# Kernel optimization log

Hardware: AMD Instinct MI355X
Metric: run time of the kernel (lower is better)

Reference implementation:

```python
import jax, jax.numpy as jnp
import numpy as np
import math

# Constants from module defaults
NUM_HEADS = 16
STEEP = 10.0        # SpikeFunction surrogate steepness
LEAK = 0.9          # LIF leak_rate
THRESH = 1.0        # spike_threshold
REFRAC = 2.0        # refractory_period
TH_DECAY = 0.95     # adaptive threshold decay

@jax.custom_vjp
def spike_fn(v, th):
    return (v >= th).astype(v.dtype)

def _spike_fwd(v, th):
    return spike_fn(v, th), (v, th)

def _spike_bwd(res, g):
    v, th = res
    s = jax.nn.sigmoid(STEEP * (v - th))
    return (g * STEEP * s * (1.0 - s), jnp.zeros_like(th))

spike_fn.defvjp(_spike_fwd, _spike_bwd)


def lif(cur_seq, W_rec, theta):
    """Leaky integrate-and-fire recurrence.
    cur_seq: [S, N, Dh] precomputed input currents (input_weights applied already).
    Returns spikes [S, N, Dh]."""
    S, N, Dh = cur_seq.shape
    dt = cur_seq.dtype
    init = (jnp.zeros((N, Dh), dt),               # membrane potential
            jnp.zeros((N, Dh), dt),               # spike history (detached)
            jnp.zeros((N, Dh), dt),               # refractory counter
            jnp.full((N, Dh), THRESH, dt))        # adaptive threshold

    def step(state, cur):
        v, hist, refrac, athr = state
        total = cur + hist @ W_rec.T
        v = LEAK * v + total
        v = v * (refrac <= 0).astype(dt)          # refractory masking
        spikes = spike_fn(v, athr)
        sm = jax.lax.stop_gradient(spikes)        # spike_mask (bool in torch, no grad)
        v = v * (1.0 - sm)                        # membrane reset
        refrac = jnp.maximum(refrac - 1.0, sm * REFRAC)
        athr = TH_DECAY * athr + sm * theta       # adaptive threshold bump
        return (v, sm, refrac, athr), spikes

    _, spikes = jax.lax.scan(step, init, cur_seq)
    return spikes


def setup_inputs() -> dict:
    key = jax.random.key(0)
    B, S, D = 4, 1024, 1024
    H = NUM_HEADS
    Dh = D // H
    ks = jax.random.split(key, 16)
    sD = 1.0 / math.sqrt(D)
    sd = 1.0 / math.sqrt(Dh)
    inp = {
        "x": jax.random.normal(ks[0], (B, S, D), jnp.float32),
        "Wq": jax.random.normal(ks[1], (D, D), jnp.float32) * sD,
        "Wk": jax.random.normal(ks[2], (D, D), jnp.float32) * sD,
        "Wv": jax.random.normal(ks[3], (D, D), jnp.float32) * sD,
        "Wo": jax.random.normal(ks[4], (D, D), jnp.float32) * sD,
        "bo": jax.random.normal(ks[5], (D,), jnp.float32) * sD,
        "Wq_in": jax.random.normal(ks[6], (Dh, Dh), jnp.float32) * sd,
        "Wq_rec": jax.random.normal(ks[7], (Dh, Dh), jnp.float32) * sd,
        "Wk_in": jax.random.normal(ks[8], (Dh, Dh), jnp.float32) * sd,
        "Wk_rec": jax.random.normal(ks[9], (Dh, Dh), jnp.float32) * sd,
        "Wv_in": jax.random.normal(ks[10], (Dh, Dh), jnp.float32) * sd,
        "Wv_rec": jax.random.normal(ks[11], (Dh, Dh), jnp.float32) * sd,
        "theta_q": jnp.full((Dh,), 0.1, jnp.float32),
        "theta_k": jnp.full((Dh,), 0.1, jnp.float32),
        "theta_v": jnp.full((Dh,), 0.1, jnp.float32),
    }
    return inp


def reference(x, Wq, Wk, Wv, Wo, bo, Wq_in, Wq_rec, Wk_in, Wk_rec,
              Wv_in, Wv_rec, theta_q, theta_k, theta_v):
    B, S, D = x.shape
    H = NUM_HEADS
    Dh = D // H

    def heads_time_major(t):
        # [B,S,D] -> [S, B*H, Dh]
        return t.reshape(B, S, H, Dh).transpose(1, 0, 2, 3).reshape(S, B * H, Dh)

    # Projections; LIF input current is linear so apply input_weights over whole seq
    cur_q = heads_time_major(x @ Wq.T) @ Wq_in.T
    cur_k = heads_time_major(x @ Wk.T) @ Wk_in.T
    cur_v = heads_time_major(x @ Wv.T) @ Wv_in.T

    qs = lif(cur_q, Wq_rec, theta_q)
    ks_ = lif(cur_k, Wk_rec, theta_k)
    vs = lif(cur_v, Wv_rec, theta_v)

    def back(t):
        # [S, B*H, Dh] -> [B, H, S, Dh]
        return t.reshape(S, B, H, Dh).transpose(1, 2, 0, 3)

    qh, kh, vh = back(qs), back(ks_), back(vs)
    scale = 1.0 / math.sqrt(Dh)
    scores = jnp.einsum('bhqd,bhkd->bhqk', qh, kh) * scale
    attn = jax.nn.softmax(scores, axis=-1)
    ctx = jnp.einsum('bhqk,bhkd->bhqd', attn, vh)
    out = ctx.transpose(0, 2, 1, 3).reshape(B, S, D) @ Wo.T + bo
    return out
```

## Files before the change

### kernel.cpp

```cpp
#include <hip/hip_runtime.h>
#include <hip/hip_bf16.h>

#define B_  4
#define S_  1024
#define D_  1024
#define H_  16
#define DH_ 64
#define N_  64
#define BS_ 4096

#define WS_CUR   0ull
#define WS_XH    (WS_CUR + 48ull*1024*1024)
#define WS_XL    (WS_XH  +  8ull*1024*1024)
#define WS_WCH   (WS_XL  +  8ull*1024*1024)
#define WS_WCL   (WS_WCH +  6ull*1024*1024)
#define WS_MSK   (WS_WCL +  6ull*1024*1024)
#define WS_CTXH  WS_XH
#define WS_CTXL  WS_XL
#define WS_WOH   WS_WCH
#define WS_WOL   (WS_WCH + 2ull*1024*1024)

typedef __attribute__((ext_vector_type(8))) short short8v;
typedef __attribute__((ext_vector_type(4))) float f32x4;

__device__ inline void bsplit(float x, unsigned short& h, unsigned short& l) {
    unsigned ux = __float_as_uint(x);
    unsigned rh = (ux + 0x7FFFu + ((ux >> 16) & 1u)) >> 16;
    h = (unsigned short)rh;
    float r = x - __uint_as_float(rh << 16);
    unsigned ur = __float_as_uint(r);
    l = (unsigned short)((ur + 0x7FFFu + ((ur >> 16) & 1u)) >> 16);
}

__global__ __launch_bounds__(256) void k_prep(
    const float* __restrict__ x,
    const float* __restrict__ Wq, const float* __restrict__ Wk, const float* __restrict__ Wv,
    const float* __restrict__ Wqi, const float* __restrict__ Wki, const float* __restrict__ Wvi,
    unsigned short* __restrict__ xh, unsigned short* __restrict__ xl,
    unsigned short* __restrict__ wch, unsigned short* __restrict__ wcl)
{
    int blk = blockIdx.x;
    int tid = threadIdx.x;

    if (blk < 4096) {
        int i = (blk * 256 + tid) * 4;
        float4 v = *reinterpret_cast<const float4*>(&x[i]);
        ushort4 h, l;
        bsplit(v.x, h.x, l.x);
        bsplit(v.y, h.y, l.y);
        bsplit(v.z, h.z, l.z);
        bsplit(v.w, h.w, l.w);
        *reinterpret_cast<ushort4*>(&xh[i]) = h;
        *reinterpret_cast<ushort4*>(&xl[i]) = l;
        return;
    }

    int q = blk - 4096;
    int z = q >> 10, hd = q & 1023;
    const float* W  = (z == 0) ? Wq  : (z == 1) ? Wk  : Wv;
    const float* Wi = (z == 0) ? Wqi : (z == 1) ? Wki : Wvi;
    int h = hd >> 6, d = hd & 63;

    __shared__ float ws[64];
    if (tid < 64) ws[tid] = Wi[d * 64 + tid];
    __syncthreads();

    const float* Wb = W + (size_t)h * 64 * 1024;
    float acc[4] = {0.f, 0.f, 0.f, 0.f};
    for (int j = 0; j < 64; j++) {
        float wv = ws[j];
        const float* row = Wb + (size_t)j * 1024;
        #pragma unroll
        for (int mi = 0; mi < 4; mi++)
            acc[mi] += row[tid + mi * 256] * wv;
    }
    unsigned short* oh = wch + (size_t)z * 1024 * 1024 + (size_t)hd * 1024;
    unsigned short* ol = wcl + (size_t)z * 1024 * 1024 + (size_t)hd * 1024;
    #pragma unroll
    for (int mi = 0; mi < 4; mi++) {
        unsigned short hh, ll;
        bsplit(acc[mi], hh, ll);
        oh[tid + mi * 256] = hh;
        ol[tid + mi * 256] = ll;
    }
}

template<int OUT>
__global__ __launch_bounds__(512, 4) void k_mfma_gemm(
    const unsigned short* __restrict__ Ah, const unsigned short* __restrict__ Al,
    const unsigned short* __restrict__ Bh, const unsigned short* __restrict__ Bl,
    float* __restrict__ C, const float* __restrict__ bias)
{
    __shared__ __align__(16) unsigned short lds[4 * 128 * 64];

    int tid = threadIdx.x;
    int bx = blockIdx.x, by = blockIdx.y, bz = blockIdx.z;
    const unsigned short* Bhz = Bh + (size_t)bz * 1024 * 1024;
    const unsigned short* Blz = Bl + (size_t)bz * 1024 * 1024;
    int rb = bx * 128, cb = by * 128;

    int wid = tid >> 6, lane = tid & 63;
    int wr = wid >> 2, wc = wid & 3;
    int r15 = lane & 15, g = lane >> 4;

    int rowA = lane >> 3;
    int kpsw = ((lane & 7) ^ rowA) * 8;

    f32x4 acc[4][2];
    #pragma unroll
    for (int mt = 0; mt < 4; mt++)
        #pragma unroll
        for (int nt = 0; nt < 2; nt++)
            acc[mt][nt] = (f32x4){0.f, 0.f, 0.f, 0.f};

    #pragma unroll 1
    for (int t = 0; t < 16; t++) {
        int kb = t * 64;
        #pragma unroll
        for (int i = 0; i < 8; i++) {
            int q = wid * 8 + i;
            int mat = q >> 4, ch = q & 15;
            const unsigned short* gsrc = (mat == 0) ? Ah : (mat == 1) ? Al
                                        : (mat == 2) ? Bhz : Blz;
            int rowoff = (mat < 2) ? rb : cb;
            int row = ch * 8 + rowA;
            __builtin_amdgcn_global_load_lds(
                (const __attribute__((address_space(1))) void*)
                    (gsrc + (size_t)(rowoff + row) * 1024 + kb + kpsw),
                (__attribute__((address_space(3))) void*)(&lds[mat * 8192 + ch * 512]),
                16, 0, 0);
        }
        __syncthreads();

        #pragma unroll
        for (int kk = 0; kk < 2; kk++) {
            short8v bh[2], bl[2];
            #pragma unroll
            for (int nt = 0; nt < 2; nt++) {
                int Crow = wc * 32 + nt * 16 + r15;
                int off = Crow * 64 + (((kk * 4 + g) ^ (Crow & 7)) * 8);
                bh[nt] = *reinterpret_cast<const short8v*>(&lds[2 * 8192 + off]);
                bl[nt] = *reinterpret_cast<const short8v*>(&lds[3 * 8192 + off]);
            }
            #pragma unroll
            for (int mt = 0; mt < 4; mt++) {
                int Arow = wr * 64 + mt * 16 + r15;
                int off = Arow * 64 + (((kk * 4 + g) ^ (Arow & 7)) * 8);
                short8v ah = *reinterpret_cast<const short8v*>(&lds[0 * 8192 + off]);
                short8v al = *reinterpret_cast<const short8v*>(&lds[1 * 8192 + off]);
                #pragma unroll
                for (int nt = 0; nt < 2; nt++) {
                    acc[mt][nt] = __builtin_amdgcn_mfma_f32_16x16x32_bf16(bh[nt], ah, acc[mt][nt], 0, 0, 0);
                    acc[mt][nt] = __builtin_amdgcn_mfma_f32_16x16x32_bf16(bl[nt], ah, acc[mt][nt], 0, 0, 0);
                    acc[mt][nt] = __builtin_amdgcn_mfma_f32_16x16x32_bf16(bh[nt], al, acc[mt][nt], 0, 0, 0);
                }
            }
        }
        __syncthreads();
    }

    if (OUT == 0) {
        float* out = C + (size_t)bz * 64 * 1024 * 64;
        int b = rb >> 10;
        #pragma unroll
        for (int nt = 0; nt < 2; nt++) {
            int col = cb + wc * 32 + nt * 16 + g * 4;
            int h = col >> 6, dd = col & 63;
            #pragma unroll
            for (int mt = 0; mt < 4; mt++) {
                int row = rb + wr * 64 + mt * 16 + r15;
                int s = row & 1023;
                f32x4 a = acc[mt][nt];
                *reinterpret_cast<float4*>(&out[(((size_t)(b * 16 + h)) * 1024 + s) * 64 + dd]) =
                    make_float4(a[0], a[1], a[2], a[3]);
            }
        }
    } else {
        #pragma unroll
        for (int nt = 0; nt < 2; nt++) {
            int col = cb + wc * 32 + nt * 16 + g * 4;
            float4 bv = *reinterpret_cast<const float4*>(&bias[col]);
            #pragma unroll
            for (int mt = 0; mt < 4; mt++) {
                int row = rb + wr * 64 + mt * 16 + r15;
                f32x4 a = acc[mt][nt];
                *reinterpret_cast<float4*>(&C[(size_t)row * 1024 + col]) =
                    make_float4(a[0] + bv.x, a[1] + bv.y, a[2] + bv.z, a[3] + bv.w);
            }
        }
    }
}

__global__ __launch_bounds__(64) void k_lif_wo(
    const float* __restrict__ curAll,
    const float* __restrict__ Wrq, const float* __restrict__ Wrk, const float* __restrict__ Wrv,
    const float* __restrict__ thq, const float* __restrict__ thk, const float* __restrict__ thv,
    unsigned long long* __restrict__ masks,
    const float* __restrict__ Wo, unsigned short* __restrict__ woh, unsigned short* __restrict__ wol)
{
    __shared__ float T[16 * 16 * 64];
    __shared__ __align__(16) float cbuf[2][64 * 64];

    int bid = blockIdx.x;
    int d = threadIdx.x;

    if (bid >= 192) {
        int q = bid - 192;
        #pragma unroll
        for (int it = 0; it < 8; it++) {
            int i = q * 2048 + it * 256 + d * 4;
            float4 v = *reinterpret_cast<const float4*>(&Wo[i]);
            ushort4 h, l;
            bsplit(v.x, h.x, l.x);
            bsplit(v.y, h.y, l.y);
            bsplit(v.z, h.z, l.z);
            bsplit(v.w, h.w, l.w);
            *reinterpret_cast<ushort4*>(&woh[i]) = h;
            *reinterpret_cast<ushort4*>(&wol[i]) = l;
        }
        return;
    }

    int l = bid >> 6, n = bid & 63;
    const float* W  = (l == 0) ? Wrq : (l == 1) ? Wrk : Wrv;
    const float* th = (l == 0) ? thq : (l == 1) ? thk : thv;
    const float* cbase = curAll + (((size_t)l * 64 + n) * 1024) * 64;
    unsigned long long* mout = masks + ((size_t)l * 64 + n) * 1024;

    #pragma unroll
    for (int j = 0; j < 16; j++)
        __builtin_amdgcn_global_load_lds(
            (const __attribute__((address_space(1))) void*)(cbase + j * 256 + d * 4),
            (__attribute__((address_space(3))) void*)(&cbuf[0][j * 256]), 16, 0, 0);

    float theta = th[d];

    for (int g = 0; g < 16; g++) {
        float w0 = W[d * 64 + 4 * g + 0];
        float w1 = W[d * 64 + 4 * g + 1];
        float w2 = W[d * 64 + 4 * g + 2];
        float w3 = W[d * 64 + 4 * g + 3];
        #pragma unroll
        for (int c = 0; c < 16; c++) {
            float t = 0.f;
            if (c & 1) t += w0;
            if (c & 2) t += w1;
            if (c & 4) t += w2;
            if (c & 8) t += w3;
            T[g * 1024 + c * 64 + d] = t;
        }
    }
    __syncthreads();

    float v = 0.f, refrac = 0.f, athr = 1.0f;
    unsigned mlo = 0u, mhi = 0u;
    unsigned bufLo = 0u, bufHi = 0u;

    for (int b = 0; b < 16; b++) {
        if (b < 15) {
            const float* src = cbase + (size_t)(b + 1) * 4096;
            float* dst = cbuf[(b + 1) & 1];
            #pragma unroll
            for (int j = 0; j < 16; j++)
                __builtin_amdgcn_global_load_lds(
                    (const __attribute__((address_space(1))) void*)(src + j * 256 + d * 4),
                    (__attribute__((address_space(3))) void*)(dst + j * 256), 16, 0, 0);
        }
        if (b == 0)      asm volatile("s_waitcnt vmcnt(16)" ::: "memory");
        else if (b < 15) asm volatile("s_waitcnt vmcnt(17)" ::: "memory");
        else             asm volatile("s_waitcnt vmcnt(0)"  ::: "memory");

        const float* cb = cbuf[b & 1];
        #pragma unroll 8
        for (int i = 0; i < 64; i++) {
            float curv = cb[i * 64 + d];

            float t[16];
            #pragma unroll
            for (int g = 0; g < 8; g++)
                t[g] = T[g * 1024 + (int)(((mlo >> (4 * g)) & 15u) << 6) + d];
            #pragma unroll
            for (int g = 0; g < 8; g++)
                t[8 + g] = T[(8 + g) * 1024 + (int)(((mhi >> (4 * g)) & 15u) << 6) + d];

            #pragma unroll
            for (int k = 8; k >= 1; k >>= 1)
                #pragma unroll
                for (int j = 0; j < k; j++)
                    t[j] = t[j] + t[j + k];
            float total = curv + t[0];

            v = 0.9f * v + total;
            v = (refrac <= 0.f) ? v : 0.f;
            bool sp = (v >= athr);
            unsigned long long m = __ballot(sp);
            mlo = (unsigned)m;
            mhi = (unsigned)(m >> 32);
            bufLo = (d == i) ? mlo : bufLo;
            bufHi = (d == i) ? mhi : bufHi;
            float sm = sp ? 1.f : 0.f;
            v = sp ? 0.f : v;
            refrac = fmaxf(refrac - 1.f, sm * 2.f);
            athr = 0.95f * athr + sm * theta;
        }
        mout[b * 64 + d] = ((unsigned long long)bufHi << 32) | bufLo;
    }
}

#define ATT_C1 0.180336879f
#define ATT_C2 11.541560327f

__device__ inline short8v expand8(unsigned byte) {
    short8v r;
    #pragma unroll
    for (int e = 0; e < 8; e++)
        r[e] = (short)(((byte >> e) & 1u) ? 0x3F80 : 0);
    return r;
}

__device__ inline unsigned bfpk(float x, float y) {
    unsigned ux = __float_as_uint(x);
    unsigned uy = __float_as_uint(y);
    unsigned rx = (ux + 0x7FFFu + ((ux >> 16) & 1u)) >> 16;
    unsigned ry = (uy + 0x7FFFu + ((uy >> 16) & 1u)) >> 16;
    return rx | (ry << 16);
}

__global__ __launch_bounds__(256) void k_attn_mfma(
    const unsigned long long* __restrict__ masks,
    unsigned short* __restrict__ ctxh, unsigned short* __restrict__ ctxl)
{
    __shared__ __align__(16) unsigned short Klds[128][72];
    __shared__ __align__(16) unsigned short Vt[64][136];
    __shared__ unsigned long long vmbuf[2][128];

    const unsigned long long* qm_all = masks;
    const unsigned long long* km_all = masks + (size_t)64 * 1024;
    const unsigned long long* vm_all = masks + (size_t)2 * 64 * 1024;

    int n  = blockIdx.y;
    int qc = blockIdx.x;
    int tid = threadIdx.x;
    int wv = tid >> 6;
    int lane = tid & 63;
    int r15 = lane & 15, g = lane >> 4;

    const unsigned long long* km = km_all + (size_t)n * 1024;
    const unsigned long long* vm = vm_all + (size_t)n * 1024;

    unsigned long long qmask = qm_all[(size_t)n * 1024 + qc * 64 + wv * 16 + r15];
    short8v Qf[2];
    #pragma unroll
    for (int ch = 0; ch < 2; ch++)
        Qf[ch] = expand8((unsigned)(qmask >> ((ch * 4 + g) * 8)) & 0xFFu);

    f32x4 cx[4];
    #pragma unroll
    for (int mt = 0; mt < 4; mt++) cx[mt] = (f32x4){0.f, 0.f, 0.f, 0.f};
    float den = 0.f;

    if (tid < 128) vmbuf[0][tid] = vm[tid];
    __syncthreads();

    for (int kt = 0; kt < 8; kt++) {
        {
            int s = tid >> 1, half = tid & 1;
            unsigned long long m = km[kt * 128 + s];
            #pragma unroll
            for (int j = 0; j < 4; j++) {
                unsigned byte = (unsigned)(m >> (half * 32 + j * 8)) & 0xFFu;
                *reinterpret_cast<short8v*>(&Klds[s][(half * 4 + j) * 8]) = expand8(byte);
            }
        }
        {
            int dh = tid & 63;
            int sc4 = tid >> 6;
            #pragma unroll
            for (int j = 0; j < 4; j++) {
                short8v v2;
                #pragma unroll
                for (int e = 0; e < 8; e++) {
                    unsigned long long mv = vmbuf[kt & 1][sc4 * 32 + j * 8 + e];
                    v2[e] = (short)(((mv >> dh) & 1ull) ? 0x3F80 : 0);
                }
                *reinterpret_cast<short8v*>(&Vt[dh][(sc4 * 4 + j) * 8]) = v2;
            }
        }
        __syncthreads();

        if (tid < 128 && kt + 1 < 8) vmbuf[(kt + 1) & 1][tid] = vm[(kt + 1) * 128 + tid];

        f32x4 pf[8];
        #pragma unroll
        for (int mt = 0; mt < 8; mt++) {
            f32x4 c = (f32x4){0.f, 0.f, 0.f, 0.f};
            #pragma unroll
            for (int ch = 0; ch < 2; ch++) {
                short8v a = *reinterpret_cast<const short8v*>(&Klds[mt * 16 + r15][(ch * 4 + g) * 8]);
                c = __builtin_amdgcn_mfma_f32_16x16x32_bf16(a, Qf[ch], c, 0, 0, 0);
            }
            f32x4 p;
            #pragma unroll
            for (int i = 0; i < 4; i++) {
                p[i] = exp2f(c[i] * ATT_C1 - ATT_C2);
                den += p[i];
            }
            pf[mt] = p;
        }

        int src0 = ((g & 1) << 1) * 16 + r15;
        int src1 = src0 + 16;
        bool hi = (g >= 2);
        #pragma unroll
        for (int c4 = 0; c4 < 4; c4++) {
            unsigned d0 = bfpk(pf[2 * c4][0], pf[2 * c4][1]);
            unsigned d1 = bfpk(pf[2 * c4][2], pf[2 * c4][3]);
            unsigned d2 = bfpk(pf[2 * c4 + 1][0], pf[2 * c4 + 1][1]);
            unsigned d3 = bfpk(pf[2 * c4 + 1][2], pf[2 * c4 + 1][3]);
            unsigned a0 = __shfl((int)d0, src0), b0 = __shfl((int)d2, src0);
            unsigned a1 = __shfl((int)d1, src0), b1 = __shfl((int)d3, src0);
            unsigned a2 = __shfl((int)d0, src1), b2 = __shfl((int)d2, src1);
            unsigned a3 = __shfl((int)d1, src1), b3 = __shfl((int)d3, src1);
            union { unsigned u[4]; short8v s; } bw;
            bw.u[0] = hi ? b0 : a0;
            bw.u[1] = hi ? b1 : a1;
            bw.u[2] = hi ? b2 : a2;
            bw.u[3] = hi ? b3 : a3;
            #pragma unroll
            for (int mt = 0; mt < 4; mt++) {
                short8v a = *reinterpret_cast<const short8v*>(&Vt[mt * 16 + r15][(c4 * 4 + g) * 8]);
                cx[mt] = __builtin_amdgcn_mfma_f32_16x16x32_bf16(a, bw.s, cx[mt], 0, 0, 0);
            }
        }
        __syncthreads();
    }

    den += __shfl_xor(den, 16);
    den += __shfl_xor(den, 32);
    float inv = 1.f / den;

    int b = n >> 4, h = n & 15;
    int row = b * 1024 + qc * 64 + wv * 16 + r15;
    unsigned short* oph = ctxh + (size_t)row * 1024 + h * 64;
    unsigned short* opl = ctxl + (size_t)row * 1024 + h * 64;
    #pragma unroll
    for (int mt = 0; mt < 4; mt++)
        #pragma unroll
        for (int i = 0; i < 4; i++) {
            unsigned short hh, ll;
            bsplit(cx[mt][i] * inv, hh, ll);
            oph[mt * 16 + g * 4 + i] = hh;
            opl[mt * 16 + g * 4 + i] = ll;
        }
}

extern "C" void kernel_launch(void* const* d_in, const int* in_sizes, int n_in,
                              void* d_out, int out_size, void* d_ws, size_t ws_size,
                              hipStream_t stream) {
    const float* x    = (const float*)d_in[0];
    const float* Wq   = (const float*)d_in[1];
    const float* Wk   = (const float*)d_in[2];
    const float* Wv   = (const float*)d_in[3];
    const float* Wo   = (const float*)d_in[4];
    const float* bo   = (const float*)d_in[5];
    const float* Wqi  = (const float*)d_in[6];
    const float* Wqr  = (const float*)d_in[7];
    const float* Wki  = (const float*)d_in[8];
    const float* Wkr  = (const float*)d_in[9];
    const float* Wvi  = (const float*)d_in[10];
    const float* Wvr  = (const float*)d_in[11];
    const float* thq  = (const float*)d_in[12];
    const float* thk  = (const float*)d_in[13];
    const float* thv  = (const float*)d_in[14];

    char* ws = (char*)d_ws;
    float* cur = (float*)(ws + WS_CUR);
    unsigned short* xh  = (unsigned short*)(ws + WS_XH);
    unsigned short* xl  = (unsigned short*)(ws + WS_XL);
    unsigned short* wch = (unsigned short*)(ws + WS_WCH);
    unsigned short* wcl = (unsigned short*)(ws + WS_WCL);
    unsigned long long* masks = (unsigned long long*)(ws + WS_MSK);
    unsigned short* ctxh = (unsigned short*)(ws + WS_CTXH);
    unsigned short* ctxl = (unsigned short*)(ws + WS_CTXL);
    unsigned short* woh = (unsigned short*)(ws + WS_WOH);
    unsigned short* wol = (unsigned short*)(ws + WS_WOL);
    float* outp = (float*)d_out;

    k_prep<<<dim3(7168, 1, 1), 256, 0, stream>>>(x, Wq, Wk, Wv, Wqi, Wki, Wvi, xh, xl, wch, wcl);
    k_mfma_gemm<0><<<dim3(32, 8, 3), 512, 0, stream>>>(xh, xl, wch, wcl, cur, nullptr);
    k_lif_wo<<<dim3(704, 1, 1), 64, 0, stream>>>(cur, Wqr, Wkr, Wvr, thq, thk, thv, masks, Wo, woh, wol);
    k_attn_mfma<<<dim3(16, 64, 1), 256, 0, stream>>>(masks, ctxh, ctxl);
    k_mfma_gemm<1><<<dim3(32, 8, 1), 512, 0, stream>>>(ctxh, ctxl, woh, wol, outp, bo);
}
```

Baseline: 411.5 us.

## Double-buffer LDS in split-bf16 MFMA GEMM with K=32 tiles and block swizzle

Restructures the GEMM main loop to use two LDS buffers with K-tiles of 32, issuing the next tile's global-to-LDS loads before computing on the current one, with explicit vmcnt waits and barriers. Block indices are remapped so blocks that run together share operand tiles in L2. A new XOR swizzle matches the narrower tile width. This hides global load latency behind MFMA work, at the cost of twice as many iterations and barriers and reliance on hand-written waitcnt ordering for correctness.

```diff
diff --git a/kernel.cpp b/kernel.cpp
--- a/kernel.cpp
+++ b/kernel.cpp
@@ -91,10 +91,14 @@
     const unsigned short* __restrict__ Bh, const unsigned short* __restrict__ Bl,
     float* __restrict__ C, const float* __restrict__ bias)
 {
-    __shared__ __align__(16) unsigned short lds[4 * 128 * 64];
+    __shared__ __align__(16) unsigned short lds[2][4][128 * 32];
 
     int tid = threadIdx.x;
-    int bx = blockIdx.x, by = blockIdx.y, bz = blockIdx.z;
+    int bz = blockIdx.z;
+    int lin = blockIdx.x + 32 * blockIdx.y;
+    int swz = (lin & 7) * 32 + (lin >> 3);
+    int bx = swz & 31, by = swz >> 5;
+
     const unsigned short* Bhz = Bh + (size_t)bz * 1024 * 1024;
     const unsigned short* Blz = Bl + (size_t)bz * 1024 * 1024;
     int rb = bx * 128, cb = by * 128;
@@ -103,8 +107,9 @@
     int wr = wid >> 2, wc = wid & 3;
     int r15 = lane & 15, g = lane >> 4;
 
-    int rowA = lane >> 3;
-    int kpsw = ((lane & 7) ^ rowA) * 8;
+    int rowL = lane >> 2;
+    int gslot = (lane & 3) ^ (rowL & 3) ^ ((rowL >> 2) & 3);
+    int fx = (r15 & 3) ^ ((r15 >> 2) & 3);
 
     f32x4 acc[4][2];
     #pragma unroll
@@ -113,50 +118,63 @@
         for (int nt = 0; nt < 2; nt++)
             acc[mt][nt] = (f32x4){0.f, 0.f, 0.f, 0.f};
 
-    #pragma unroll 1
-    for (int t = 0; t < 16; t++) {
-        int kb = t * 64;
-        #pragma unroll
-        for (int i = 0; i < 8; i++) {
-            int q = wid * 8 + i;
-            int mat = q >> 4, ch = q & 15;
+    auto issue = [&](int t, int buf) {
+        int kb = t * 32;
+        #pragma unroll
+        for (int i = 0; i < 4; i++) {
+            int q = wid * 4 + i;
+            int mat = q >> 3, ch = q & 7;
             const unsigned short* gsrc = (mat == 0) ? Ah : (mat == 1) ? Al
                                         : (mat == 2) ? Bhz : Blz;
             int rowoff = (mat < 2) ? rb : cb;
-            int row = ch * 8 + rowA;
+            int row = ch * 16 + rowL;
             __builtin_amdgcn_global_load_lds(
                 (const __attribute__((address_space(1))) void*)
-                    (gsrc + (size_t)(rowoff + row) * 1024 + kb + kpsw),
-                (__attribute__((address_space(3))) void*)(&lds[mat * 8192 + ch * 512]),
+                    (gsrc + (size_t)(rowoff + row) * 1024 + kb + gslot * 8),
+                (__attribute__((address_space(3))) void*)(&lds[buf][mat][ch * 512]),
                 16, 0, 0);
         }
-        __syncthreads();
-
-        #pragma unroll
-        for (int kk = 0; kk < 2; kk++) {
-            short8v bh[2], bl[2];
+    };
+
+    auto compute = [&](int buf) {
+        const unsigned short* L0 = lds[buf][0];
+        const unsigned short* L1 = lds[buf][1];
+        const unsigned short* L2 = lds[buf][2];
+        const unsigned short* L3 = lds[buf][3];
+        short8v bh[2], bl[2];
+        #pragma unroll
+        for (int nt = 0; nt < 2; nt++) {
+            int Crow = wc * 32 + nt * 16 + r15;
+            int off = Crow * 32 + ((g ^ fx) * 8);
+            bh[nt] = *reinterpret_cast<const short8v*>(&L2[off]);
+            bl[nt] = *reinterpret_cast<const short8v*>(&L3[off]);
+        }
+        #pragma unroll
+        for (int mt = 0; mt < 4; mt++) {
+            int Arow = wr * 64 + mt * 16 + r15;
+            int off = Arow * 32 + ((g ^ fx) * 8);
+            short8v ah = *reinterpret_cast<const short8v*>(&L0[off]);
+            short8v al = *reinterpret_cast<const short8v*>(&L1[off]);
             #pragma unroll
             for (int nt = 0; nt < 2; nt++) {
-                int Crow = wc * 32 + nt * 16 + r15;
-                int off = Crow * 64 + (((kk * 4 + g) ^ (Crow & 7)) * 8);
-                bh[nt] = *reinterpret_cast<const short8v*>(&lds[2 * 8192 + off]);
-                bl[nt] = *reinterpret_cast<const short8v*>(&lds[3 * 8192 + off]);
-            }
-            #pragma unroll
-            for (int mt = 0; mt < 4; mt++) {
-                int Arow = wr * 64 + mt * 16 + r15;
-                int off = Arow * 64 + (((kk * 4 + g) ^ (Arow & 7)) * 8);
-                short8v ah = *reinterpret_cast<const short8v*>(&lds[0 * 8192 + off]);
-                short8v al = *reinterpret_cast<const short8v*>(&lds[1 * 8192 + off]);
-                #pragma unroll
-                for (int nt = 0; nt < 2; nt++) {
-                    acc[mt][nt] = __builtin_amdgcn_mfma_f32_16x16x32_bf16(bh[nt], ah, acc[mt][nt], 0, 0, 0);
-                    acc[mt][nt] = __builtin_amdgcn_mfma_f32_16x16x32_bf16(bl[nt], ah, acc[mt][nt], 0, 0, 0);
-                    acc[mt][nt] = __builtin_amdgcn_mfma_f32_16x16x32_bf16(bh[nt], al, acc[mt][nt], 0, 0, 0);
-                }
-            }
-        }
-        __syncthreads();
+                acc[mt][nt] = __builtin_amdgcn_mfma_f32_16x16x32_bf16(bh[nt], ah, acc[mt][nt], 0, 0, 0);
+                acc[mt][nt] = __builtin_amdgcn_mfma_f32_16x16x32_bf16(bl[nt], ah, acc[mt][nt], 0, 0, 0);
+                acc[mt][nt] = __builtin_amdgcn_mfma_f32_16x16x32_bf16(bh[nt], al, acc[mt][nt], 0, 0, 0);
+            }
+        }
+    };
+
+    issue(0, 0);
+    #pragma unroll 1
+    for (int t = 0; t < 32; t++) {
+        if (t < 31) {
+            issue(t + 1, (t + 1) & 1);
+            asm volatile("s_waitcnt vmcnt(4)\n\ts_barrier" ::: "memory");
+        } else {
+            asm volatile("s_waitcnt vmcnt(0)\n\ts_barrier" ::: "memory");
+        }
+        compute(t & 1);
+        asm volatile("s_barrier" ::: "memory");
     }
 
     if (OUT == 0) {
```

After: 428.5 us. 4.1% more time.

## Interleave two independent LIF recurrences per wave to hide serial latency

Applied to the files above, without the earlier changes.

Each LIF wave now runs two independent head sequences, A and B, in one time loop. Their lookup-table LDS reads, reductions and ballots are interleaved, so the dependency chains can overlap instead of stalling on each step's latency. The number of LIF blocks is halved and the Wo-split blocks are renumbered. The double-buffered current tiles are duplicated and the wait logic is simplified. This raises LDS use per block and register pressure, and puts half as many waves in flight across the CUs.

```diff
diff --git a/kernel.cpp b/kernel.cpp
--- a/kernel.cpp
+++ b/kernel.cpp
@@ -199,13 +199,14 @@
     const float* __restrict__ Wo, unsigned short* __restrict__ woh, unsigned short* __restrict__ wol)
 {
     __shared__ float T[16 * 16 * 64];
-    __shared__ __align__(16) float cbuf[2][64 * 64];
+    __shared__ __align__(16) float cbufA[2][4096];
+    __shared__ __align__(16) float cbufB[2][4096];
 
     int bid = blockIdx.x;
     int d = threadIdx.x;
 
-    if (bid >= 192) {
-        int q = bid - 192;
+    if (bid >= 96) {
+        int q = bid - 96;
         #pragma unroll
         for (int it = 0; it < 8; it++) {
             int i = q * 2048 + it * 256 + d * 4;
@@ -221,17 +222,25 @@
         return;
     }
 
-    int l = bid >> 6, n = bid & 63;
+    int l = bid >> 5, q = bid & 31;
+    int nA = q * 2, nB = q * 2 + 1;
     const float* W  = (l == 0) ? Wrq : (l == 1) ? Wrk : Wrv;
     const float* th = (l == 0) ? thq : (l == 1) ? thk : thv;
-    const float* cbase = curAll + (((size_t)l * 64 + n) * 1024) * 64;
-    unsigned long long* mout = masks + ((size_t)l * 64 + n) * 1024;
+    const float* cbaseA = curAll + (((size_t)l * 64 + nA) * 1024) * 64;
+    const float* cbaseB = curAll + (((size_t)l * 64 + nB) * 1024) * 64;
+    unsigned long long* moutA = masks + ((size_t)l * 64 + nA) * 1024;
+    unsigned long long* moutB = masks + ((size_t)l * 64 + nB) * 1024;
 
     #pragma unroll
     for (int j = 0; j < 16; j++)
         __builtin_amdgcn_global_load_lds(
-            (const __attribute__((address_space(1))) void*)(cbase + j * 256 + d * 4),
-            (__attribute__((address_space(3))) void*)(&cbuf[0][j * 256]), 16, 0, 0);
+            (const __attribute__((address_space(1))) void*)(cbaseA + j * 256 + d * 4),
+            (__attribute__((address_space(3))) void*)(&cbufA[0][j * 256]), 16, 0, 0);
+    #pragma unroll
+    for (int j = 0; j < 16; j++)
+        __builtin_amdgcn_global_load_lds(
+            (const __attribute__((address_space(1))) void*)(cbaseB + j * 256 + d * 4),
+            (__attribute__((address_space(3))) void*)(&cbufB[0][j * 256]), 16, 0, 0);
 
     float theta = th[d];
 
@@ -252,58 +261,91 @@
     }
     __syncthreads();
 
-    float v = 0.f, refrac = 0.f, athr = 1.0f;
-    unsigned mlo = 0u, mhi = 0u;
-    unsigned bufLo = 0u, bufHi = 0u;
+    float vA = 0.f, refracA = 0.f, athrA = 1.0f;
+    float vB = 0.f, refracB = 0.f, athrB = 1.0f;
+    unsigned mloA = 0u, mhiA = 0u, mloB = 0u, mhiB = 0u;
+    unsigned bufLoA = 0u, bufHiA = 0u, bufLoB = 0u, bufHiB = 0u;
 
     for (int b = 0; b < 16; b++) {
+        if (b) asm volatile("s_waitcnt vmcnt(2)" ::: "memory");
         if (b < 15) {
-            const float* src = cbase + (size_t)(b + 1) * 4096;
-            float* dst = cbuf[(b + 1) & 1];
+            const float* srcA = cbaseA + (size_t)(b + 1) * 4096;
+            const float* srcB = cbaseB + (size_t)(b + 1) * 4096;
+            float* dstA = cbufA[(b + 1) & 1];
+            float* dstB = cbufB[(b + 1) & 1];
             #pragma unroll
             for (int j = 0; j < 16; j++)
                 __builtin_amdgcn_global_load_lds(
-                    (const __attribute__((address_space(1))) void*)(src + j * 256 + d * 4),
-                    (__attribute__((address_space(3))) void*)(dst + j * 256), 16, 0, 0);
-        }
-        if (b == 0)      asm volatile("s_waitcnt vmcnt(16)" ::: "memory");
-        else if (b < 15) asm volatile("s_waitcnt vmcnt(17)" ::: "memory");
-        else             asm volatile("s_waitcnt vmcnt(0)"  ::: "memory");
-
-        const float* cb = cbuf[b & 1];
-        #pragma unroll 8
+                    (const __attribute__((address_space(1))) void*)(srcA + j * 256 + d * 4),
+                    (__attribute__((address_space(3))) void*)(dstA + j * 256), 16, 0, 0);
+            #pragma unroll
+            for (int j = 0; j < 16; j++)
+                __builtin_amdgcn_global_load_lds(
+                    (const __attribute__((address_space(1))) void*)(srcB + j * 256 + d * 4),
+                    (__attribute__((address_space(3))) void*)(dstB + j * 256), 16, 0, 0);
+        }
+
+        const float* cbA = cbufA[b & 1];
+        const float* cbB = cbufB[b & 1];
+        #pragma unroll 4
         for (int i = 0; i < 64; i++) {
-            float curv = cb[i * 64 + d];
-
-            float t[16];
+            float curA = cbA[i * 64 + d];
+            float curB = cbB[i * 64 + d];
+
+            float tA[16], tB[16];
             #pragma unroll
             for (int g = 0; g < 8; g++)
-                t[g] = T[g * 1024 + (int)(((mlo >> (4 * g)) & 15u) << 6) + d];
+                tA[g] = T[g * 1024 + (int)(((mloA >> (4 * g)) & 15u) << 6) + d];
             #pragma unroll
             for (int g = 0; g < 8; g++)
-                t[8 + g] = T[(8 + g) * 1024 + (int)(((mhi >> (4 * g)) & 15u) << 6) + d];
+                tA[8 + g] = T[(8 + g) * 1024 + (int)(((mhiA >> (4 * g)) & 15u) << 6) + d];
+            #pragma unroll
+            for (int g = 0; g < 8; g++)
+                tB[g] = T[g * 1024 + (int)(((mloB >> (4 * g)) & 15u) << 6) + d];
+            #pragma unroll
+            for (int g = 0; g < 8; g++)
+                tB[8 + g] = T[(8 + g) * 1024 + (int)(((mhiB >> (4 * g)) & 15u) << 6) + d];
 
             #pragma unroll
             for (int k = 8; k >= 1; k >>= 1)
                 #pragma unroll
                 for (int j = 0; j < k; j++)
-                    t[j] = t[j] + t[j + k];
-            float total = curv + t[0];
-
-            v = 0.9f * v + total;
-            v = (refrac <= 0.f) ? v : 0.f;
-            bool sp = (v >= athr);
-            unsigned long long m = __ballot(sp);
-            mlo = (unsigned)m;
-            mhi = (unsigned)(m >> 32);
-            bufLo = (d == i) ? mlo : bufLo;
-            bufHi = (d == i) ? mhi : bufHi;
-            float sm = sp ? 1.f : 0.f;
-            v = sp ? 0.f : v;
-            refrac = fmaxf(refrac - 1.f, sm * 2.f);
-            athr = 0.95f * athr + sm * theta;
-        }
-        mout[b * 64 + d] = ((unsigned long long)bufHi << 32) | bufLo;
+                    tA[j] = tA[j] + tA[j + k];
+            float totalA = curA + tA[0];
+            vA = 0.9f * vA + totalA;
+            vA = (refracA <= 0.f) ? vA : 0.f;
+            bool spA = (vA >= athrA);
+            unsigned long long mA = __ballot(spA);
+            mloA = (unsigned)mA;
+            mhiA = (unsigned)(mA >> 32);
+            bufLoA = (d == i) ? mloA : bufLoA;
+            bufHiA = (d == i) ? mhiA : bufHiA;
+            float smA = spA ? 1.f : 0.f;
+            vA = spA ? 0.f : vA;
+            refracA = fmaxf(refracA - 1.f, smA * 2.f);
+            athrA = 0.95f * athrA + smA * theta;
+
+            #pragma unroll
+            for (int k = 8; k >= 1; k >>= 1)
+                #pragma unroll
+                for (int j = 0; j < k; j++)
+                    tB[j] = tB[j] + tB[j + k];
+            float totalB = curB + tB[0];
+            vB = 0.9f * vB + totalB;
+            vB = (refracB <= 0.f) ? vB : 0.f;
+            bool spB = (vB >= athrB);
+            unsigned long long mB = __ballot(spB);
+            mloB = (unsigned)mB;
+            mhiB = (unsigned)(mB >> 32);
+            bufLoB = (d == i) ? mloB : bufLoB;
+            bufHiB = (d == i) ? mhiB : bufHiB;
+            float smB = spB ? 1.f : 0.f;
+            vB = spB ? 0.f : vB;
+            refracB = fmaxf(refracB - 1.f, smB * 2.f);
+            athrB = 0.95f * athrB + smB * theta;
+        }
+        moutA[b * 64 + d] = ((unsigned long long)bufHiA << 32) | bufLoA;
+        moutB[b * 64 + d] = ((unsigned long long)bufHiB << 32) | bufLoB;
     }
 }
 
@@ -488,7 +530,7 @@
 
     k_prep<<<dim3(7168, 1, 1), 256, 0, stream>>>(x, Wq, Wk, Wv, Wqi, Wki, Wvi, xh, xl, wch, wcl);
     k_mfma_gemm<0><<<dim3(32, 8, 3), 512, 0, stream>>>(xh, xl, wch, wcl, cur, nullptr);
-    k_lif_wo<<<dim3(704, 1, 1), 64, 0, stream>>>(cur, Wqr, Wkr, Wvr, thq, thk, thv, masks, Wo, woh, wol);
+    k_lif_wo<<<dim3(608, 1, 1), 64, 0, stream>>>(cur, Wqr, Wkr, Wvr, thq, thk, thv, masks, Wo, woh, wol);
     k_attn_mfma<<<dim3(16, 64, 1), 256, 0, stream>>>(masks, ctxh, ctxl);
     k_mfma_gemm<1><<<dim3(32, 8, 1), 512, 0, stream>>>(ctxh, ctxl, woh, wol, outp, bo);
 }
```

Result: slower. 560.8 us (+36.3%).
